# Kernel tuning notes

Measured on AMD Instinct MI355X. Metric: run time of the kernel, lower is better.

Reference implementation:

```python
import jax, jax.numpy as jnp
import numpy as np

K = 3          # patch_size
PAD = 1        # (K-1)//2
EPS = 1e-8
STYLE_STRENGTH = 1.0


def _whiten(x):
    # WCT whitening: zero-mean, multiply by Cov^{-1/2} (eigendecomposition)
    B, C, H, W = x.shape
    f = x.reshape(B, C, H * W)
    f = f - f.mean(-1, keepdims=True)
    cov = jnp.einsum('bcn,bdn->bcd', f, f) / (H * W - 1)
    e, v = jnp.linalg.eigh(cov)
    d = 1.0 / jnp.sqrt(jnp.maximum(e, EPS))
    wmat = jnp.einsum('bce,be,bde->bcd', v, d, v)   # V diag(e^-1/2) V^T
    return jnp.einsum('bcd,bdn->bcn', wmat, f).reshape(B, C, H, W)


def _color(x, target):
    # WCT coloring: multiply by style Cov^{1/2}, add style mean
    B, C, H, W = x.shape
    f = x.reshape(B, C, H * W)
    t = target.reshape(B, C, -1)
    tm = t.mean(-1, keepdims=True)
    tc = t - tm
    cov = jnp.einsum('bcn,bdn->bcd', tc, tc) / (tc.shape[-1] - 1)
    e, v = jnp.linalg.eigh(cov)
    d = jnp.sqrt(jnp.maximum(e, 0.0))
    cmat = jnp.einsum('bce,be,bde->bcd', v, d, v)   # V diag(e^1/2) V^T
    out = jnp.einsum('bcd,bdn->bcn', cmat, f) + tm
    return out.reshape(B, C, H, W)


def _extract_patches(x):
    # [B,C,H,W] -> [B,H*W,C,K*K], zero padding, stride 1 (matches torch unfold order)
    B, C, H, W = x.shape
    xp = jnp.pad(x, ((0, 0), (0, 0), (PAD, PAD), (PAD, PAD)))
    pats = jnp.stack([xp[:, :, i:i + H, j:j + W] for i in range(K) for j in range(K)], axis=-1)
    return pats.reshape(B, C, H * W, K * K).transpose(0, 2, 1, 3)


def _style_decorator(content_feature, style_feature):
    nc = _whiten(content_feature)
    ns = _whiten(style_feature)
    B, C, H, W = nc.shape
    P = ns.shape[2] * ns.shape[3]                     # number of style patches
    kern = _extract_patches(ns).reshape(B, P, C * K * K)
    knorm = jnp.linalg.norm(kern, axis=2, keepdims=True) + 1e-5
    cpat = _extract_patches(nc).reshape(B, H * W, C * K * K)
    # conv2d with normalized style kernels == cosine-similarity cross-correlation
    score = jnp.einsum('bqm,bpm->bpq', cpat, kern / knorm)    # [B, P, H*W]
    # binarization_patch_score: per-pixel argmax over style patches (one-hot),
    # then deconv with UNNORMALIZED kernels == gather the winning kernel per pixel
    idx = jnp.argmax(score, axis=1)                           # [B, H*W]
    gathered = jnp.take_along_axis(kern, idx[:, :, None], axis=1)  # [B, H*W, C*K*K]
    G = gathered.reshape(B, H, W, C, K, K).transpose(0, 3, 1, 2, 4, 5)  # [B,C,H,W,K,K]
    # conv_transpose2d(pad=K-1) on zero-padded one-hot == overlap-add of kernels
    full = jnp.zeros((B, C, H + K - 1, W + K - 1), dtype=nc.dtype)
    for dx in range(K):
        for dy in range(K):
            full = full.at[:, :, dx:dx + H, dy:dy + W].add(G[..., dx, dy])
    out = full[:, :, PAD:PAD + H, PAD:PAD + W]
    # norm_deconvolution: overlap counts (static)
    nfull = np.zeros((H + K - 1, W + K - 1), dtype=np.float32)
    for dx in range(K):
        for dy in range(K):
            nfull[dx:dx + H, dy:dy + W] += 1.0
    dn = jnp.asarray(nfull[PAD:PAD + H, PAD:PAD + W])
    reassembled = out / dn
    stylized = _color(reassembled, style_feature)
    return (1.0 - STYLE_STRENGTH) * content_feature + STYLE_STRENGTH * stylized


def setup_inputs() -> dict:
    key = jax.random.key(0)
    k1, k2 = jax.random.split(key)
    return {
        'content_feature': jax.random.normal(k1, (2, 512, 64, 64), dtype=jnp.float32),
        'style_feature': jax.random.normal(k2, (2, 512, 64, 64), dtype=jnp.float32),
    }


def reference(content_feature, style_feature):
    return _style_decorator(content_feature, style_feature)
```

## Files before the change

kernel.cpp:

```cpp
#include <hip/hip_runtime.h>


#define CH    512
#define NPIX  4096
#define HPAD  66
#define PPAD  4356
#define MROWS 4480
#define S0W   4480
#define NS_ITERS 7

typedef unsigned short u16;
typedef _Float16 half8 __attribute__((ext_vector_type(8)));
typedef __attribute__((ext_vector_type(4))) float f32x4;

__device__ __forceinline__ float f16tof(u16 h){
  union { u16 u; _Float16 f; } v; v.u = h; return (float)v.f;
}
__device__ __forceinline__ void split2(float x, u16& h, u16& l){
  _Float16 hf = (_Float16)x;
  float r = (x - (float)hf) * 2048.0f;
  union { u16 u; _Float16 f; } hv, lv;
  hv.f = hf; lv.f = (_Float16)r;
  h = hv.u; l = lv.u;
}
__device__ __forceinline__ void gll16(const void* g, void* l){
  __builtin_amdgcn_global_load_lds((const __attribute__((address_space(1))) unsigned*)g,
                                   (__attribute__((address_space(3))) unsigned*)l,
                                   16, 0, 0);
}
__device__ __forceinline__ f32x4 mfma_f16(half8 a, half8 b, f32x4 c){
  return __builtin_amdgcn_mfma_f32_16x16x32_f16(a, b, c, 0, 0, 0);
}

enum { M_COVP = 0, M_NST = 1, M_X3 = 2, M_WHITEN = 3, M_S0 = 4, M_COLOR = 5 };

struct GP {
  const u16 *Ah, *Al, *Bh, *Bl;
  const u16 *Eh, *El, *Fh, *Fl;
  size_t sAz, sBz;
  float* Cf;
  u16 *Ch, *Cl;
  u16 *Gh, *Gl;
  size_t sCz;
  const float* scales;
  const float* meanv;
  int K;
  int Kit;
};

template<int TILE, int MODE, int KSTEP = 32>
__global__ __launch_bounds__(256, 2)
void gemm_sp(GP p){
  constexpr int MF = TILE / 32;
  constexpr int SLOTS = KSTEP / 8;
  constexpr int TSUB = KSTEP / 32;
  constexpr bool SYM = (MODE == M_NST) || (MODE == M_X3);
  int z = blockIdx.z;
  int m0, n0;
  int kbase = 0;
  int za = z, zout = z;
  bool mirror = false;
  if constexpr (MODE == M_COVP){
    const int b = blockIdx.x;
    const int xcd = b & 7, w = b >> 3;
    const int zc = xcd*2 + (w & 1);
    const int tile = w >> 1;
    m0 = (tile >> 3)*64; n0 = (tile & 7)*64;
    kbase = (zc & 3) * p.Kit;
    za = zc >> 2; zout = zc;
  } else if constexpr (SYM){
    int bx = blockIdx.x;
    int ty = 0;
    while((ty+1)*(ty+2)/2 <= bx) ++ty;
    int tx = bx - ty*(ty+1)/2;
    m0 = ty*64; n0 = tx*64; mirror = (tx != ty);
  } else if constexpr (MODE == M_S0){
    const int b = blockIdx.x;
    const int x = b & 7, w = b >> 3;
    const int R = (x < 3) ? 5 : 4;
    if(w >= R*35) return;
    const int g   = w / (R*7);
    const int rem = w - g*(R*7);
    const int mi = rem / 7, ni = rem % 7;
    m0 = (x + mi*8) * 128;
    n0 = (g*7 + ni) * 128;
  } else if constexpr (MODE == M_WHITEN){
    const int b = blockIdx.x;
    const int x = b & 7, w = b >> 3;
    z = x >> 1;
    const int mt = (x & 1) + (w >> 2) * 2;
    m0 = mt * 128;
    n0 = (w & 3) * 128;
    za = z; zout = z;
  } else {
    m0 = blockIdx.y*TILE; n0 = blockIdx.x*TILE;
  }

  const u16 *Ah, *Al, *Bh, *Bl;
  if constexpr (MODE == M_X3){
    const size_t zb = (size_t)(z & 3) * CH * CH;
    if(z < 4){ Ah=p.Ah+zb; Al=p.Al+zb; Bh=p.Bh+zb; Bl=p.Bl+zb; }
    else     { Ah=p.Eh+zb; Al=p.El+zb; Bh=p.Fh+zb; Bl=p.Fl+zb; }
  } else {
    Ah = p.Ah + (size_t)za * p.sAz;
    Al = p.Al + (size_t)za * p.sAz;
    Bh = p.Bh + (size_t)za * p.sBz;
    Bl = p.Bl + (size_t)za * p.sBz;
  }

  const int tid = threadIdx.x, ln = tid & 63, wv = tid >> 6;
  const int wm = (wv >> 1) * (TILE/2), wn = (wv & 1) * (TILE/2);
  __shared__ __align__(16) u16 sAh[2][TILE*KSTEP], sAl[2][TILE*KSTEP];
  __shared__ __align__(16) u16 sBh[2][TILE*KSTEP], sBl[2][TILE*KSTEP];
  f32x4 acc1[MF][MF], acc2[MF][MF];
#pragma unroll
  for(int i=0;i<MF;++i)
#pragma unroll
    for(int j=0;j<MF;++j){ acc1[i][j] = (f32x4)0.0f; acc2[i][j] = (f32x4)0.0f; }
  const int K = p.K;

  auto stage = [&](int k0, int buf){
#pragma unroll
    for(int s = tid; s < TILE*SLOTS; s += 256){
      const int row = s / SLOTS, pos = s % SLOTS;
      const int kc = pos ^ ((row >> 2) & (SLOTS-1));
      const size_t ga = (size_t)(m0 + row) * K + k0 + kc*8;
      const size_t gb = (size_t)(n0 + row) * K + k0 + kc*8;
      gll16(Ah + ga, sAh[buf] + s*8);
      gll16(Al + ga, sAl[buf] + s*8);
      gll16(Bh + gb, sBh[buf] + s*8);
      gll16(Bl + gb, sBl[buf] + s*8);
    }
  };

  stage(kbase, 0);
  int cur = 0;
  for(int kk = 0; kk < p.Kit; kk += KSTEP){
    __syncthreads();
    if(kk + KSTEP < p.Kit) stage(kbase + kk + KSTEP, cur ^ 1);
    const u16* pAh = sAh[cur]; const u16* pAl = sAl[cur];
    const u16* pBh = sBh[cur]; const u16* pBl = sBl[cur];
#pragma unroll
    for(int t = 0; t < TSUB; ++t){
      half8 ah[MF], al[MF], bh[MF], bl[MF];
#pragma unroll
      for(int i=0;i<MF;++i){
        const int ra = wm + i*16 + (ln & 15);
        const int rb = wn + i*16 + (ln & 15);
        const int pa = (t*4 + (ln >> 4)) ^ ((ra >> 2) & (SLOTS-1));
        const int pb = (t*4 + (ln >> 4)) ^ ((rb >> 2) & (SLOTS-1));
        const int ofa = ra*KSTEP + pa*8;
        const int ofb = rb*KSTEP + pb*8;
        ah[i] = *(const half8*)(pAh + ofa);
        al[i] = *(const half8*)(pAl + ofa);
        bh[i] = *(const half8*)(pBh + ofb);
        bl[i] = *(const half8*)(pBl + ofb);
      }
#pragma unroll
      for(int i=0;i<MF;++i)
#pragma unroll
        for(int j=0;j<MF;++j){
          acc1[i][j] = mfma_f16(ah[i], bh[j], acc1[i][j]);
          acc2[i][j] = mfma_f16(ah[i], bl[j], acc2[i][j]);
          acc2[i][j] = mfma_f16(al[i], bh[j], acc2[i][j]);
        }
    }
    cur ^= 1;
  }
  u16 *C0 = nullptr, *C1 = nullptr;
  if constexpr (MODE == M_NST){
    const size_t zb = (size_t)z * p.sCz;
    C0 = p.Ch + zb; C1 = p.Cl + zb;
  } else if constexpr (MODE == M_X3){
    const size_t zb = (size_t)(z & 3) * p.sCz;
    if(z < 4){ C0 = p.Ch + zb; C1 = p.Cl + zb; }
    else     { C0 = p.Gh + zb; C1 = p.Gl + zb; }
  }
#pragma unroll
  for(int i=0;i<MF;++i)
#pragma unroll
    for(int j=0;j<MF;++j)
#pragma unroll
      for(int r=0;r<4;++r){
        const int m = m0 + wm + i*16 + (ln >> 4)*4 + r;
        const int n = n0 + wn + j*16 + (ln & 15);
        float v = acc1[i][j][r] + acc2[i][j][r] * (1.0f/2048.0f);
        if constexpr (MODE == M_COVP){
          p.Cf[(size_t)zout * p.sCz + (size_t)m * CH + n] = v;
        } else if constexpr (MODE == M_NST || MODE == M_X3){
          if constexpr (MODE == M_NST) v = -0.5f*v + ((m == n) ? 1.5f : 0.0f);
          u16 h, l; split2(v, h, l);
          C0[(size_t)m*CH + n] = h; C1[(size_t)m*CH + n] = l;
          if(mirror){
            C0[(size_t)n*CH + m] = h; C1[(size_t)n*CH + m] = l;
          }
        } else if constexpr (MODE == M_WHITEN){
          v *= p.scales[z*4 + 3];
          const int prow = ((m >> 6) + 1)*HPAD + (m & 63) + 1;
          u16 h, l; split2(v, h, l);
          const size_t o = (size_t)z*p.sCz + (size_t)prow*CH + n;
          p.Ch[o] = h; p.Cl[o] = l;
        } else if constexpr (MODE == M_S0){
          p.Cf[(size_t)m * S0W + n] = v;
        } else {
          const float sc = p.scales[(2+z)*4 + 2];
          const float mu = p.meanv[(2+z)*CH + m];
          p.Cf[(size_t)z*p.sCz + (size_t)m*NPIX + n] = v*sc + mu;
        }
      }
}

__global__ __launch_bounds__(256)
void cov_reduce_kernel(const float* __restrict__ covp, float* __restrict__ cov,
                       float* __restrict__ rowsum){
  size_t t = (size_t)blockIdx.x * 256 + threadIdx.x;
  int z = (int)(t >> 18);
  size_t e = t & 262143;
  float s = 0.f;
#pragma unroll
  for(int c = 0; c < 4; ++c) s += covp[((size_t)(z*4 + c) << 18) + e];
  s *= (1.0f / 4095.0f);
  cov[t] = s;
  __shared__ float red[256];
  red[threadIdx.x] = fabsf(s); __syncthreads();
  for(int w = 128; w > 0; w >>= 1){
    if(threadIdx.x < w) red[threadIdx.x] += red[threadIdx.x + w];
    __syncthreads();
  }
  if(threadIdx.x == 0){
    int row = (int)(e >> 9);
    atomicAdd(&rowsum[z*512 + row], red[0]);
  }
}

__global__ __launch_bounds__(256)
void scale_fin_kernel(const float* __restrict__ rowsum, float* __restrict__ scales){
  __shared__ float red[256];
  for(int z = 0; z < 4; ++z){
    float m = fmaxf(rowsum[z*512 + threadIdx.x], rowsum[z*512 + 256 + threadIdx.x]);
    red[threadIdx.x] = m; __syncthreads();
    for(int w = 128; w > 0; w >>= 1){
      if(threadIdx.x < w) red[threadIdx.x] = fmaxf(red[threadIdx.x], red[threadIdx.x + w]);
      __syncthreads();
    }
    if(threadIdx.x == 0){
      float c = red[0];
      scales[z*4+0] = c;
      scales[z*4+1] = 1.0f / c;
      scales[z*4+2] = sqrtf(c);
      scales[z*4+3] = rsqrtf(c);
    }
    __syncthreads();
  }
}

__global__ __launch_bounds__(256)
void mean_kernel(const float* __restrict__ content, const float* __restrict__ style,
                 float* __restrict__ meanv){
  int mm = blockIdx.x;
  int z = mm >> 9, c = mm & 511;
  const float* X = ((z < 2) ? content + (size_t)z * CH * NPIX
                            : style   + (size_t)(z - 2) * CH * NPIX) + (size_t)c * NPIX;
  float s = 0.f;
  for(int i = threadIdx.x; i < NPIX; i += 256) s += X[i];
  __shared__ float red[256];
  red[threadIdx.x] = s; __syncthreads();
  for(int w = 128; w > 0; w >>= 1){
    if(threadIdx.x < w) red[threadIdx.x] += red[threadIdx.x + w];
    __syncthreads();
  }
  if(threadIdx.x == 0) meanv[mm] = red[0] * (1.0f / NPIX);
}

__global__ __launch_bounds__(256)
void center_split_kernel(const float* __restrict__ content, const float* __restrict__ style,
                         const float* __restrict__ meanv,
                         u16* __restrict__ Xch, u16* __restrict__ Xcl,
                         u16* __restrict__ XcTh, u16* __restrict__ XcTl){
  int z = blockIdx.z;
  const float* X = (z < 2) ? content + (size_t)z * CH * NPIX
                           : style   + (size_t)(z - 2) * CH * NPIX;
  int p0 = blockIdx.x * 64, c0 = blockIdx.y * 64;
  __shared__ float T[64][65];
  int col = threadIdx.x & 63, rq = threadIdx.x >> 6;
#pragma unroll
  for(int i = 0; i < 16; ++i){
    int r = i*4 + rq;
    int c = c0 + r;
    float v = X[(size_t)c * NPIX + p0 + col] - meanv[z*CH + c];
    u16 h, l; split2(v, h, l);
    size_t o = (size_t)(z*CH + c) * NPIX + p0 + col;
    Xch[o] = h; Xcl[o] = l;
    T[col][r] = v;
  }
  __syncthreads();
#pragma unroll
  for(int i = 0; i < 16; ++i){
    int r = i*4 + rq;
    float v = T[r][col];
    u16 h, l; split2(v, h, l);
    size_t o = (size_t)(z*NPIX + p0 + r) * CH + c0 + col;
    XcTh[o] = h; XcTl[o] = l;
  }
}

__global__ __launch_bounds__(256)
void ns_init_kernel(const float* __restrict__ cov, const float* __restrict__ scales,
                    u16* Yh, u16* Yl, u16* Zh, u16* Zl){
  size_t t = (size_t)blockIdx.x * 256 + threadIdx.x;
  int z = (int)(t >> 18);
  size_t e = t & 262143;
  int row = (int)(e >> 9), col = (int)(e & 511);
  float v = cov[t] * scales[z*4+1];
  u16 h, l; split2(v, h, l);
  Yh[t] = h; Yl[t] = l;
  Zh[t] = (row == col) ? (u16)0x3C00 : (u16)0;
  Zl[t] = 0;
}

__global__ __launch_bounds__(256)
void cn2_kernel(const u16* __restrict__ Wh, const u16* __restrict__ Wl,
                float* __restrict__ cn2){
  int b = blockIdx.y;
  int row = blockIdx.x * 16 + (threadIdx.x >> 4);
  int t = threadIdx.x & 15;
  float s = 0.f;
  if(row < PPAD){
    size_t base = ((size_t)(2 + b) * MROWS + row) * CH;
    for(int ch = t; ch < 64; ch += 16){
      uint4 hv = *(const uint4*)(Wh + base + ch*8);
      uint4 lv = *(const uint4*)(Wl + base + ch*8);
      const unsigned* hw = (const unsigned*)&hv;
      const unsigned* lw = (const unsigned*)&lv;
#pragma unroll
      for(int w = 0; w < 4; ++w){
        float v0 = f16tof((u16)(hw[w] & 0xFFFF)) + f16tof((u16)(lw[w] & 0xFFFF))*(1.0f/2048.0f);
        float v1 = f16tof((u16)(hw[w] >> 16))    + f16tof((u16)(lw[w] >> 16))*(1.0f/2048.0f);
        s = fmaf(v0, v0, s); s = fmaf(v1, v1, s);
      }
    }
  }
  for(int off = 8; off; off >>= 1) s += __shfl_down(s, off, 16);
  if(t == 0 && row < PPAD) cn2[b*PPAD + row] = s;
}

__global__ __launch_bounds__(256)
void rnorm_kernel(const float* __restrict__ cn2, float* __restrict__ rnorm){
  int b = blockIdx.y;
  int p = blockIdx.x * 256 + threadIdx.x;
  int py = p >> 6, px = p & 63;
  const float* c2 = cn2 + (size_t)b * PPAD + (size_t)py * HPAD + px;
  float s = 0.f;
#pragma unroll
  for(int i = 0; i < 3; ++i)
#pragma unroll
    for(int j = 0; j < 3; ++j) s += c2[i * HPAD + j];
  rnorm[b * 4096 + p] = 1.0f / (sqrtf(s) + 1e-5f);
}

__device__ __forceinline__ unsigned long long score_key(float s, int p){
  unsigned u = __float_as_uint(s);
  u = (u & 0x80000000u) ? ~u : (u | 0x80000000u);
  return ((unsigned long long)u << 32) | (unsigned long long)(0xFFFFFFFFu - (unsigned)p);
}

__global__ __launch_bounds__(256)
void score_partial_kernel(const float* __restrict__ S0T, const float* __restrict__ rnorm,
                          unsigned long long* __restrict__ skey, int b){
  const int blk = blockIdx.x;
  const int xcd = blk & 7, w = blk >> 3;
  const int chunk = xcd*8 + (w & 7);
  const int qg = w >> 3;
  const int t = threadIdx.x;
  const int q0 = qg*512 + t, q1 = q0 + 256;
  const int qc0 = (q0 >> 6)*HPAD + (q0 & 63);
  const int qc1 = (q1 >> 6)*HPAD + (q1 & 63);
  const float* rn = rnorm + b * 4096;
  float b0 = -1e30f, b1 = -1e30f; int i0 = 0, i1 = 0;
  for(int p = chunk*64; p < chunk*64 + 64; ++p){
    const size_t base = (size_t)((p >> 6)*HPAD + (p & 63)) * S0W;
    float s0 = 0.f, s1 = 0.f;
#pragma unroll
    for(int i = 0; i < 3; ++i)
#pragma unroll
      for(int j = 0; j < 3; ++j){
        const size_t d = (size_t)(i*HPAD + j) * (S0W + 1);
        s0 += S0T[base + qc0 + d];
        s1 += S0T[base + qc1 + d];
      }
    const float r = rn[p];
    s0 *= r; s1 *= r;
    if(s0 > b0){ b0 = s0; i0 = p; }
    if(s1 > b1){ b1 = s1; i1 = p; }
  }
  atomicMax(skey + (size_t)b*4096 + q0, score_key(b0, i0));
  atomicMax(skey + (size_t)b*4096 + q1, score_key(b1, i1));
}

__global__ __launch_bounds__(256)
void gather_kernel(const u16* __restrict__ Wh, const u16* __restrict__ Wl,
                   const unsigned long long* __restrict__ skey,
                   u16* __restrict__ RTh, u16* __restrict__ RTl){
  int g = blockIdx.x * 256 + threadIdx.x;
  int cg = g & 63;
  int pix = (g >> 6) & 4095;
  int b = g >> 18;
  int y = pix >> 6, x = pix & 63;
  const unsigned long long* kb = skey + (size_t)b * 4096;
  size_t matbase = (size_t)(2 + b) * MROWS * CH;
  float a8[8] = {0,0,0,0,0,0,0,0};
  int cnt = 0;
#pragma unroll
  for(int i = 0; i < 3; ++i){
    int qy = y + 1 - i;
    if((unsigned)qy >= 64u) continue;
#pragma unroll
    for(int j = 0; j < 3; ++j){
      int qx = x + 1 - j;
      if((unsigned)qx >= 64u) continue;
      int p = (int)(0xFFFFFFFFu - (unsigned)(kb[qy * 64 + qx] & 0xFFFFFFFFull));
      int row = ((p >> 6) + i) * HPAD + (p & 63) + j;
      size_t off = matbase + (size_t)row * CH + cg * 8;
      uint4 hv = *(const uint4*)(Wh + off);
      uint4 lv = *(const uint4*)(Wl + off);
      const unsigned* hw = (const unsigned*)&hv;
      const unsigned* lw = (const unsigned*)&lv;
#pragma unroll
      for(int w = 0; w < 4; ++w){
        a8[2*w]   += f16tof((u16)(hw[w] & 0xFFFF)) + f16tof((u16)(lw[w] & 0xFFFF))*(1.0f/2048.0f);
        a8[2*w+1] += f16tof((u16)(hw[w] >> 16))    + f16tof((u16)(lw[w] >> 16))*(1.0f/2048.0f);
      }
      ++cnt;
    }
  }
  float inv = 1.0f / (float)cnt;
  u16 oh[8], ol[8];
#pragma unroll
  for(int k = 0; k < 8; ++k){
    float v = a8[k] * inv;
    split2(v, oh[k], ol[k]);
  }
  size_t ro = ((size_t)(b * 4096 + pix)) * CH + cg * 8;
  *(uint4*)(RTh + ro) = *(const uint4*)oh;
  *(uint4*)(RTl + ro) = *(const uint4*)ol;
}

extern "C" void kernel_launch(void* const* d_in, const int* in_sizes, int n_in,
                              void* d_out, int out_size, void* d_ws, size_t ws_size,
                              hipStream_t stream){
  (void)in_sizes; (void)n_in; (void)out_size; (void)ws_size;
  const float* content = (const float*)d_in[0];
  const float* style   = (const float*)d_in[1];
  float* out = (float*)d_out;

  char* base = (char*)d_ws;
  size_t off = 0;
  auto take = [&](size_t nbytes) -> char* {
    char* p = base + off;
    off = (off + nbytes + 255) & ~(size_t)255;
    return p;
  };
  const size_t MAT = (size_t)CH*CH*2;
  const size_t FEAT = (size_t)CH*NPIX*2;
  const size_t WMAT = (size_t)MROWS*CH*2;
  const size_t S0SZ = (size_t)MROWS*S0W*4;

  float* meanv  = (float*)take((size_t)4*CH*sizeof(float));
  float* scales = (float*)take(256);
  float* rowsum = (float*)take((size_t)4*CH*sizeof(float));
  float* cov    = (float*)take((size_t)4*CH*CH*sizeof(float));
  u16 *Yh=(u16*)take(4*MAT), *Yl=(u16*)take(4*MAT);
  u16 *Zh=(u16*)take(4*MAT), *Zl=(u16*)take(4*MAT);
  u16 *Th=(u16*)take(4*MAT), *Tl=(u16*)take(4*MAT);
  u16 *Ynh=(u16*)take(4*MAT), *Ynl=(u16*)take(4*MAT);
  u16 *Znh=(u16*)take(4*MAT), *Znl=(u16*)take(4*MAT);
  float* covp = (float*)Yh;
  char* P1 = take(2*(size_t)4*WMAT);
  u16 *Xch=(u16*)P1, *Xcl=(u16*)(P1+4*FEAT);
  u16 *Wh=(u16*)P1,  *Wl=(u16*)(P1+4*WMAT);
  char* P0 = take(S0SZ);
  u16 *XcTh=(u16*)P0, *XcTl=(u16*)(P0+4*FEAT);
  float* S0T = (float*)P0;
  u16 *RTh=(u16*)P0, *RTl=(u16*)(P0+2*FEAT);
  float* cn2    = (float*)take((size_t)2*PPAD*sizeof(float));
  float* rnormb = (float*)take((size_t)2*4096*sizeof(float));
  unsigned long long* skey = (unsigned long long*)take((size_t)2*4096*8);

  hipMemsetAsync(rowsum, 0, (size_t)4*CH*sizeof(float), stream);
  hipMemsetAsync(skey, 0, (size_t)2*4096*8, stream);

  mean_kernel<<<2048, 256, 0, stream>>>(content, style, meanv);
  center_split_kernel<<<dim3(64, 8, 4), 256, 0, stream>>>(content, style, meanv,
                                                          Xch, Xcl, XcTh, XcTl);
  {
    GP g{}; g.Ah=Xch; g.Al=Xcl; g.Bh=Xch; g.Bl=Xcl;
    g.sAz = g.sBz = (size_t)CH*NPIX; g.Cf = covp; g.sCz = (size_t)CH*CH;
    g.K = NPIX; g.Kit = 1024;
    gemm_sp<64, M_COVP, 32><<<dim3(1024), 256, 0, stream>>>(g);
  }
  cov_reduce_kernel<<<4096, 256, 0, stream>>>(covp, cov, rowsum);
  scale_fin_kernel<<<1, 256, 0, stream>>>(rowsum, scales);
  ns_init_kernel<<<4096, 256, 0, stream>>>(cov, scales, Yh, Yl, Zh, Zl);

  u16 *Ach[2]={Yh,Yl}, *Bch[2]={Zh,Zl}, *An[2]={Ynh,Ynl}, *Bn[2]={Znh,Znl};
  for(int it = 0; it < NS_ITERS; ++it){
    GP t{}; t.Ah=Bch[0]; t.Al=Bch[1];
    t.Bh=Ach[0]; t.Bl=Ach[1];
    t.sAz = t.sBz = (size_t)CH*CH; t.Ch=Th; t.Cl=Tl; t.sCz=(size_t)CH*CH;
    t.K = CH; t.Kit = CH;
    gemm_sp<64, M_NST, 64><<<dim3(36, 1, 4), 256, 0, stream>>>(t);
    GP u{}; u.Ah=Ach[0]; u.Al=Ach[1];
    u.Bh=Th; u.Bl=Tl;
    u.Eh=Th; u.El=Tl;
    u.Fh=Bch[0]; u.Fl=Bch[1];
    u.Ch=An[0]; u.Cl=An[1];
    u.Gh=Bn[0]; u.Gl=Bn[1];
    u.sCz=(size_t)CH*CH; u.K = CH; u.Kit = CH;
    gemm_sp<64, M_X3, 64><<<dim3(36, 1, 8), 256, 0, stream>>>(u);
    for(int c = 0; c < 2; ++c){ u16* tmp=Ach[c]; Ach[c]=An[c]; An[c]=tmp;
                                tmp=Bch[c]; Bch[c]=Bn[c]; Bn[c]=tmp; }
  }

  hipMemsetAsync(Wh, 0, 4*WMAT, stream);
  hipMemsetAsync(Wl, 0, 4*WMAT, stream);
  {
    GP w{}; w.Ah=XcTh; w.Al=XcTl; w.sAz=(size_t)NPIX*CH;
    w.Bh=Bch[0]; w.Bl=Bch[1]; w.sBz=(size_t)CH*CH;
    w.Ch=Wh; w.Cl=Wl; w.sCz=(size_t)MROWS*CH; w.scales=scales;
    w.K = CH; w.Kit = CH;
    gemm_sp<128, M_WHITEN, 32><<<dim3(512), 256, 0, stream>>>(w);
  }
  cn2_kernel<<<dim3(273, 2), 256, 0, stream>>>(Wh, Wl, cn2);
  rnorm_kernel<<<dim3(16, 2), 256, 0, stream>>>(cn2, rnormb);

  for(int b = 0; b < 2; ++b){
    GP s{};
    s.Ah = Wh + (size_t)(2+b)*MROWS*CH; s.Al = Wl + (size_t)(2+b)*MROWS*CH;
    s.Bh = Wh + (size_t)b*MROWS*CH;     s.Bl = Wl + (size_t)b*MROWS*CH;
    s.sAz = s.sBz = 0; s.Cf = S0T; s.sCz = 0; s.K = CH; s.Kit = CH;
    gemm_sp<128, M_S0, 32><<<dim3(1400), 256, 0, stream>>>(s);
    score_partial_kernel<<<dim3(512), 256, 0, stream>>>(S0T, rnormb, skey, b);
  }

  gather_kernel<<<2048, 256, 0, stream>>>(Wh, Wl, skey, RTh, RTl);
  {
    GP c{}; c.Ah = Ach[0] + 2*(size_t)CH*CH; c.Al = Ach[1] + 2*(size_t)CH*CH;
    c.sAz = (size_t)CH*CH;
    c.Bh = RTh; c.Bl = RTl; c.sBz = (size_t)NPIX*CH;
    c.Cf = out; c.sCz = (size_t)CH*NPIX; c.scales = scales; c.meanv = meanv;
    c.K = CH; c.Kit = CH;
    gemm_sp<128, M_COLOR, 32><<<dim3(32, 4, 2), 256, 0, stream>>>(c);
  }
}
```

Before: 732.3 us.

## Fuse Newton-Schulz iterations into one persistent kernel with grid barriers

```diff
diff --git a/kernel.cpp b/kernel.cpp
--- a/kernel.cpp
+++ b/kernel.cpp
@@ -8,6 +8,8 @@
 #define MROWS 4480
 #define S0W   4480
 #define NS_ITERS 7
+#define NS_BLOCKS 288
+#define MATE  262144
 
 typedef unsigned short u16;
 typedef _Float16 half8 __attribute__((ext_vector_type(8)));
@@ -54,12 +56,10 @@
   constexpr int MF = TILE / 32;
   constexpr int SLOTS = KSTEP / 8;
   constexpr int TSUB = KSTEP / 32;
-  constexpr bool SYM = (MODE == M_NST) || (MODE == M_X3);
   int z = blockIdx.z;
   int m0, n0;
   int kbase = 0;
   int za = z, zout = z;
-  bool mirror = false;
   if constexpr (MODE == M_COVP){
     const int b = blockIdx.x;
     const int xcd = b & 7, w = b >> 3;
@@ -68,21 +68,20 @@
     m0 = (tile >> 3)*64; n0 = (tile & 7)*64;
     kbase = (zc & 3) * p.Kit;
     za = zc >> 2; zout = zc;
-  } else if constexpr (SYM){
-    int bx = blockIdx.x;
-    int ty = 0;
-    while((ty+1)*(ty+2)/2 <= bx) ++ty;
-    int tx = bx - ty*(ty+1)/2;
-    m0 = ty*64; n0 = tx*64; mirror = (tx != ty);
   } else if constexpr (MODE == M_S0){
     const int b = blockIdx.x;
-    const int x = b & 7, w = b >> 3;
-    const int R = (x < 3) ? 5 : 4;
-    if(w >= R*35) return;
-    const int g   = w / (R*7);
-    const int rem = w - g*(R*7);
+    const int x = b & 7;
+    int rem = b >> 3;
+    int g = 0, R = 0, mo = 0;
+    for(; g < 5; ++g){
+      mo = (x + 3*g) & 7;
+      R = (mo < 3) ? 5 : 4;
+      if(rem < R*7) break;
+      rem -= R*7;
+    }
+    if(g == 5) return;
     const int mi = rem / 7, ni = rem % 7;
-    m0 = (x + mi*8) * 128;
+    m0 = (mo + mi*8) * 128;
     n0 = (g*7 + ni) * 128;
   } else if constexpr (MODE == M_WHITEN){
     const int b = blockIdx.x;
@@ -97,16 +96,10 @@
   }
 
   const u16 *Ah, *Al, *Bh, *Bl;
-  if constexpr (MODE == M_X3){
-    const size_t zb = (size_t)(z & 3) * CH * CH;
-    if(z < 4){ Ah=p.Ah+zb; Al=p.Al+zb; Bh=p.Bh+zb; Bl=p.Bl+zb; }
-    else     { Ah=p.Eh+zb; Al=p.El+zb; Bh=p.Fh+zb; Bl=p.Fl+zb; }
-  } else {
-    Ah = p.Ah + (size_t)za * p.sAz;
-    Al = p.Al + (size_t)za * p.sAz;
-    Bh = p.Bh + (size_t)za * p.sBz;
-    Bl = p.Bl + (size_t)za * p.sBz;
-  }
+  Ah = p.Ah + (size_t)za * p.sAz;
+  Al = p.Al + (size_t)za * p.sAz;
+  Bh = p.Bh + (size_t)za * p.sBz;
+  Bl = p.Bl + (size_t)za * p.sBz;
 
   const int tid = threadIdx.x, ln = tid & 63, wv = tid >> 6;
   const int wm = (wv >> 1) * (TILE/2), wn = (wv & 1) * (TILE/2);
@@ -167,15 +160,6 @@
     }
     cur ^= 1;
   }
-  u16 *C0 = nullptr, *C1 = nullptr;
-  if constexpr (MODE == M_NST){
-    const size_t zb = (size_t)z * p.sCz;
-    C0 = p.Ch + zb; C1 = p.Cl + zb;
-  } else if constexpr (MODE == M_X3){
-    const size_t zb = (size_t)(z & 3) * p.sCz;
-    if(z < 4){ C0 = p.Ch + zb; C1 = p.Cl + zb; }
-    else     { C0 = p.Gh + zb; C1 = p.Gl + zb; }
-  }
 #pragma unroll
   for(int i=0;i<MF;++i)
 #pragma unroll
@@ -187,13 +171,6 @@
         float v = acc1[i][j][r] + acc2[i][j][r] * (1.0f/2048.0f);
         if constexpr (MODE == M_COVP){
           p.Cf[(size_t)zout * p.sCz + (size_t)m * CH + n] = v;
-        } else if constexpr (MODE == M_NST || MODE == M_X3){
-          if constexpr (MODE == M_NST) v = -0.5f*v + ((m == n) ? 1.5f : 0.0f);
-          u16 h, l; split2(v, h, l);
-          C0[(size_t)m*CH + n] = h; C1[(size_t)m*CH + n] = l;
-          if(mirror){
-            C0[(size_t)n*CH + m] = h; C1[(size_t)n*CH + m] = l;
-          }
         } else if constexpr (MODE == M_WHITEN){
           v *= p.scales[z*4 + 3];
           const int prow = ((m >> 6) + 1)*HPAD + (m & 63) + 1;
@@ -208,6 +185,142 @@
           p.Cf[(size_t)z*p.sCz + (size_t)m*NPIX + n] = v*sc + mu;
         }
       }
+}
+
+struct NSP {
+  u16 *Y0h, *Y0l, *Z0h, *Z0l;
+  u16 *Y1h, *Y1l, *Z1h, *Z1l;
+  u16 *Th, *Tl;
+  int* bar;
+};
+
+__device__ __forceinline__ void gbar(int* bar, int idx, int nblk){
+  __syncthreads();
+  if(threadIdx.x == 0){
+    __threadfence();
+    __hip_atomic_fetch_add(&bar[idx], 1, __ATOMIC_RELEASE, __HIP_MEMORY_SCOPE_AGENT);
+    while(__hip_atomic_load(&bar[idx], __ATOMIC_ACQUIRE, __HIP_MEMORY_SCOPE_AGENT) < nblk){
+      __builtin_amdgcn_s_sleep(16);
+    }
+  }
+  __syncthreads();
+  __threadfence();
+}
+
+__global__ __launch_bounds__(256, 2)
+void ns_persistent(NSP p){
+  const int b = blockIdx.x;
+  const int tid = threadIdx.x, ln = tid & 63, wv = tid >> 6;
+  const int wm = (wv >> 1) * 32, wn = (wv & 1) * 32;
+  __shared__ __align__(16) u16 sAh[2][64*64], sAl[2][64*64];
+  __shared__ __align__(16) u16 sBh[2][64*64], sBl[2][64*64];
+
+  const int tile = b % 36;
+  int ty = 0;
+  while((ty+1)*(ty+2)/2 <= tile) ++ty;
+  const int tx = tile - ty*(ty+1)/2;
+  const int m0 = ty*64, n0 = tx*64;
+  const bool mirror = (tx != ty);
+
+  auto run_tile = [&](const u16* Ah, const u16* Al, const u16* Bh, const u16* Bl,
+                      f32x4 (&acc1)[2][2], f32x4 (&acc2)[2][2]){
+#pragma unroll
+    for(int i=0;i<2;++i)
+#pragma unroll
+      for(int j=0;j<2;++j){ acc1[i][j] = (f32x4)0.0f; acc2[i][j] = (f32x4)0.0f; }
+    auto stage = [&](int k0, int buf){
+#pragma unroll
+      for(int s = tid; s < 512; s += 256){
+        const int row = s >> 3, pos = s & 7;
+        const int kc = pos ^ ((row >> 2) & 7);
+        const size_t ga = (size_t)(m0 + row) * CH + k0 + kc*8;
+        const size_t gb = (size_t)(n0 + row) * CH + k0 + kc*8;
+        gll16(Ah + ga, sAh[buf] + s*8);
+        gll16(Al + ga, sAl[buf] + s*8);
+        gll16(Bh + gb, sBh[buf] + s*8);
+        gll16(Bl + gb, sBl[buf] + s*8);
+      }
+    };
+    stage(0, 0);
+    int cur = 0;
+    for(int kk = 0; kk < 512; kk += 64){
+      __syncthreads();
+      if(kk + 64 < 512) stage(kk + 64, cur ^ 1);
+      const u16* pAh = sAh[cur]; const u16* pAl = sAl[cur];
+      const u16* pBh = sBh[cur]; const u16* pBl = sBl[cur];
+#pragma unroll
+      for(int t = 0; t < 2; ++t){
+        half8 ah[2], al[2], bh[2], bl[2];
+#pragma unroll
+        for(int i=0;i<2;++i){
+          const int ra = wm + i*16 + (ln & 15);
+          const int rb = wn + i*16 + (ln & 15);
+          const int pa = (t*4 + (ln >> 4)) ^ ((ra >> 2) & 7);
+          const int pb = (t*4 + (ln >> 4)) ^ ((rb >> 2) & 7);
+          ah[i] = *(const half8*)(pAh + ra*64 + pa*8);
+          al[i] = *(const half8*)(pAl + ra*64 + pa*8);
+          bh[i] = *(const half8*)(pBh + rb*64 + pb*8);
+          bl[i] = *(const half8*)(pBl + rb*64 + pb*8);
+        }
+#pragma unroll
+        for(int i=0;i<2;++i)
+#pragma unroll
+          for(int j=0;j<2;++j){
+            acc1[i][j] = mfma_f16(ah[i], bh[j], acc1[i][j]);
+            acc2[i][j] = mfma_f16(ah[i], bl[j], acc2[i][j]);
+            acc2[i][j] = mfma_f16(al[i], bh[j], acc2[i][j]);
+          }
+      }
+      cur ^= 1;
+    }
+  };
+
+  auto store_tile = [&](u16* C0, u16* C1, bool isT,
+                        f32x4 (&acc1)[2][2], f32x4 (&acc2)[2][2]){
+#pragma unroll
+    for(int i=0;i<2;++i)
+#pragma unroll
+      for(int j=0;j<2;++j)
+#pragma unroll
+        for(int r=0;r<4;++r){
+          const int m = m0 + wm + i*16 + (ln >> 4)*4 + r;
+          const int n = n0 + wn + j*16 + (ln & 15);
+          float v = acc1[i][j][r] + acc2[i][j][r] * (1.0f/2048.0f);
+          if(isT) v = -0.5f*v + ((m == n) ? 1.5f : 0.0f);
+          u16 h, l; split2(v, h, l);
+          C0[(size_t)m*CH + n] = h; C1[(size_t)m*CH + n] = l;
+          if(mirror){
+            C0[(size_t)n*CH + m] = h; C1[(size_t)n*CH + m] = l;
+          }
+        }
+  };
+
+  f32x4 a1[2][2], a2[2][2];
+  for(int it = 0; it < NS_ITERS; ++it){
+    const bool par = it & 1;
+    u16* sYh = par ? p.Y1h : p.Y0h;  u16* sYl = par ? p.Y1l : p.Y0l;
+    u16* sZh = par ? p.Z1h : p.Z0h;  u16* sZl = par ? p.Z1l : p.Z0l;
+    u16* dYh = par ? p.Y0h : p.Y1h;  u16* dYl = par ? p.Y0l : p.Y1l;
+    u16* dZh = par ? p.Z0h : p.Z1h;  u16* dZl = par ? p.Z0l : p.Z1l;
+    if(b < 144){
+      const size_t zb = (size_t)(b / 36) * MATE;
+      run_tile(sZh + zb, sZl + zb, sYh + zb, sYl + zb, a1, a2);
+      store_tile(p.Th + zb, p.Tl + zb, true, a1, a2);
+    }
+    gbar(p.bar, it*2, NS_BLOCKS);
+    {
+      const int z8 = b / 36;
+      const size_t zb = (size_t)(z8 & 3) * MATE;
+      if(z8 < 4){
+        run_tile(sYh + zb, sYl + zb, p.Th + zb, p.Tl + zb, a1, a2);
+        store_tile(dYh + zb, dYl + zb, false, a1, a2);
+      } else {
+        run_tile(p.Th + zb, p.Tl + zb, sZh + zb, sZl + zb, a1, a2);
+        store_tile(dZh + zb, dZl + zb, false, a1, a2);
+      }
+    }
+    gbar(p.bar, it*2 + 1, NS_BLOCKS);
+  }
 }
 
 __global__ __launch_bounds__(256)
@@ -485,9 +598,11 @@
   float* cn2    = (float*)take((size_t)2*PPAD*sizeof(float));
   float* rnormb = (float*)take((size_t)2*4096*sizeof(float));
   unsigned long long* skey = (unsigned long long*)take((size_t)2*4096*8);
+  int* nsbar = (int*)take(64);
 
   hipMemsetAsync(rowsum, 0, (size_t)4*CH*sizeof(float), stream);
   hipMemsetAsync(skey, 0, (size_t)2*4096*8, stream);
+  hipMemsetAsync(nsbar, 0, 64, stream);
 
   mean_kernel<<<2048, 256, 0, stream>>>(content, style, meanv);
   center_split_kernel<<<dim3(64, 8, 4), 256, 0, stream>>>(content, style, meanv,
@@ -496,36 +611,25 @@
     GP g{}; g.Ah=Xch; g.Al=Xcl; g.Bh=Xch; g.Bl=Xcl;
     g.sAz = g.sBz = (size_t)CH*NPIX; g.Cf = covp; g.sCz = (size_t)CH*CH;
     g.K = NPIX; g.Kit = 1024;
-    gemm_sp<64, M_COVP, 32><<<dim3(1024), 256, 0, stream>>>(g);
+    gemm_sp<64, M_COVP, 64><<<dim3(1024), 256, 0, stream>>>(g);
   }
   cov_reduce_kernel<<<4096, 256, 0, stream>>>(covp, cov, rowsum);
   scale_fin_kernel<<<1, 256, 0, stream>>>(rowsum, scales);
   ns_init_kernel<<<4096, 256, 0, stream>>>(cov, scales, Yh, Yl, Zh, Zl);
 
-  u16 *Ach[2]={Yh,Yl}, *Bch[2]={Zh,Zl}, *An[2]={Ynh,Ynl}, *Bn[2]={Znh,Znl};
-  for(int it = 0; it < NS_ITERS; ++it){
-    GP t{}; t.Ah=Bch[0]; t.Al=Bch[1];
-    t.Bh=Ach[0]; t.Bl=Ach[1];
-    t.sAz = t.sBz = (size_t)CH*CH; t.Ch=Th; t.Cl=Tl; t.sCz=(size_t)CH*CH;
-    t.K = CH; t.Kit = CH;
-    gemm_sp<64, M_NST, 64><<<dim3(36, 1, 4), 256, 0, stream>>>(t);
-    GP u{}; u.Ah=Ach[0]; u.Al=Ach[1];
-    u.Bh=Th; u.Bl=Tl;
-    u.Eh=Th; u.El=Tl;
-    u.Fh=Bch[0]; u.Fl=Bch[1];
-    u.Ch=An[0]; u.Cl=An[1];
-    u.Gh=Bn[0]; u.Gl=Bn[1];
-    u.sCz=(size_t)CH*CH; u.K = CH; u.Kit = CH;
-    gemm_sp<64, M_X3, 64><<<dim3(36, 1, 8), 256, 0, stream>>>(u);
-    for(int c = 0; c < 2; ++c){ u16* tmp=Ach[c]; Ach[c]=An[c]; An[c]=tmp;
-                                tmp=Bch[c]; Bch[c]=Bn[c]; Bn[c]=tmp; }
+  {
+    NSP n{};
+    n.Y0h=Yh; n.Y0l=Yl; n.Z0h=Zh; n.Z0l=Zl;
+    n.Y1h=Ynh; n.Y1l=Ynl; n.Z1h=Znh; n.Z1l=Znl;
+    n.Th=Th; n.Tl=Tl; n.bar=nsbar;
+    ns_persistent<<<dim3(NS_BLOCKS), 256, 0, stream>>>(n);
   }
 
   hipMemsetAsync(Wh, 0, 4*WMAT, stream);
   hipMemsetAsync(Wl, 0, 4*WMAT, stream);
   {
     GP w{}; w.Ah=XcTh; w.Al=XcTl; w.sAz=(size_t)NPIX*CH;
-    w.Bh=Bch[0]; w.Bl=Bch[1]; w.sBz=(size_t)CH*CH;
+    w.Bh=Znh; w.Bl=Znl; w.sBz=(size_t)CH*CH;
     w.Ch=Wh; w.Cl=Wl; w.sCz=(size_t)MROWS*CH; w.scales=scales;
     w.K = CH; w.Kit = CH;
     gemm_sp<128, M_WHITEN, 32><<<dim3(512), 256, 0, stream>>>(w);
@@ -538,13 +642,13 @@
     s.Ah = Wh + (size_t)(2+b)*MROWS*CH; s.Al = Wl + (size_t)(2+b)*MROWS*CH;
     s.Bh = Wh + (size_t)b*MROWS*CH;     s.Bl = Wl + (size_t)b*MROWS*CH;
     s.sAz = s.sBz = 0; s.Cf = S0T; s.sCz = 0; s.K = CH; s.Kit = CH;
-    gemm_sp<128, M_S0, 32><<<dim3(1400), 256, 0, stream>>>(s);
+    gemm_sp<128, M_S0, 32><<<dim3(1232), 256, 0, stream>>>(s);
     score_partial_kernel<<<dim3(512), 256, 0, stream>>>(S0T, rnormb, skey, b);
   }
 
   gather_kernel<<<2048, 256, 0, stream>>>(Wh, Wl, skey, RTh, RTl);
   {
-    GP c{}; c.Ah = Ach[0] + 2*(size_t)CH*CH; c.Al = Ach[1] + 2*(size_t)CH*CH;
+    GP c{}; c.Ah = Ynh + 2*(size_t)CH*CH; c.Al = Ynl + 2*(size_t)CH*CH;
     c.sAz = (size_t)CH*CH;
     c.Bh = RTh; c.Bl = RTl; c.sBz = (size_t)NPIX*CH;
     c.Cf = out; c.sCz = (size_t)CH*NPIX; c.scales = scales; c.meanv = meanv;
```

Result: slower. 1.807 ms (+146.7%).
